# Kernel optimization log

Measured on AMD Instinct MI355X. Metric: run time of the kernel, lower is better.

The kernel has to match this reference:

```python
import jax, jax.numpy as jnp
import numpy as np

B, GRID, WIDTH, NBLOCKS = 128, 32, 100, 50  # num_layers=100 -> 50 two-GEMM residual blocks


def _forward(inputs, W0, Wa, Wb, b1, b2, b3, b4, mult, Wout, bout):
    Bb, G = inputs.shape[0], inputs.shape[1]
    T = G // 2
    even = jnp.arange(0, G, 2)
    odd = even + 1
    idx = (even - 1) % G  # [(i-1) % G for even i]

    def patch(i1, i2):
        # gather axis1 then axis2 -> (B, T, T, 3, 3) flattened to (B*T*T, 9)
        return inputs[:, i1][:, :, i2].reshape(-1, 9)

    # order: right, left, up, down, center (matches tf.concat order)
    flat = jnp.concatenate([patch(odd, even), patch(idx, even), patch(even, odd),
                            patch(even, idx), patch(even, even)], axis=-1)  # (B*T*T, 45)

    x = jax.nn.relu(flat @ W0)  # (B*T*T, 100)

    def block(x, p):
        wa, wb, bb1, bb2, bb3, bb4, m = p
        x1 = (x + bb1) @ wa
        x1 = 2.0 * x1 + bb2          # x1 + bias_2 + x1
        x1 = jax.nn.relu(x1)
        x1 = 2.0 * x1 + bb3          # x1 + bias_3 + x1
        x1 = (x1 @ wb) * m
        x = jax.nn.relu(x + x1 + bb4)
        return x, None

    x, _ = jax.lax.scan(block, x, (Wa, Wb, b1, b2, b3, b4, mult))

    x = (x @ Wout + bout).reshape(Bb, T, T, 4)

    jp1 = (jnp.arange(T) + 1) % T
    jm1 = (jnp.arange(T) - 1) % T
    x0, x1c, x2, x3 = x[..., 0], x[..., 1], x[..., 2], x[..., 3]
    right_c = x0 / (x1c[:, jp1] + x0)
    left_c = x1c / (x1c + x0[:, jm1])
    up_c = x2 / (x2 + x3[:, :, jp1])
    down_c = x3 / (x2[:, :, jm1] + x3)

    # corner contributions from the original fine-grid stencils
    oo = inputs[:, odd][:, :, odd]    # odd-odd fine points (ru corner)
    oi = inputs[:, odd][:, :, idx]    # rd corner
    io = inputs[:, idx][:, :, odd]    # lu corner
    ii = inputs[:, idx][:, :, idx]    # ld corner
    ru = -(oo[..., 0, 0] + oo[..., 1, 0] * right_c + oo[..., 0, 1] * up_c) / oo[..., 1, 1]
    rd = -(oi[..., 0, 2] + oi[..., 1, 2] * right_c + oi[..., 0, 1] * down_c) / oi[..., 1, 1]
    lu = -(io[..., 2, 0] + io[..., 1, 0] * left_c + io[..., 2, 1] * up_c) / io[..., 1, 1]
    ld = -(ii[..., 2, 2] + ii[..., 1, 2] * left_c + ii[..., 2, 1] * down_c) / ii[..., 1, 1]

    ones = jnp.ones_like(down_c)
    first_row = jnp.stack([ld, left_c, lu], axis=-1)
    second_row = jnp.stack([down_c, ones, up_c], axis=-1)
    third_row = jnp.stack([rd, right_c, ru], axis=-1)
    out = jnp.stack([first_row, second_row, third_row], axis=0)  # (3, B, T, T, 3)
    return jnp.transpose(out, (1, 2, 3, 0, 4))  # (B, T, T, 3, 3)


def setup_inputs() -> dict:
    key = jax.random.key(0)
    ks = jax.random.split(key, 6)
    # positive stencil entries keep the corner divisions well-conditioned
    inputs = jax.random.uniform(ks[0], (B, GRID, GRID, 3, 3), jnp.float32) + 0.5
    W0 = jax.random.normal(ks[1], (45, WIDTH), jnp.float32) * np.float32(np.sqrt(2.0 / 45))
    Wa = jax.random.normal(ks[2], (NBLOCKS, WIDTH, WIDTH), jnp.float32) * np.float32(np.sqrt(2.0 / WIDTH))
    # original inits linear_{i+1} to zeros; small random keeps the baseline non-degenerate
    Wb = jax.random.normal(ks[3], (NBLOCKS, WIDTH, WIDTH), jnp.float32) * np.float32(0.01)
    b1 = jnp.zeros((NBLOCKS,), jnp.float32)
    b2 = jnp.zeros((NBLOCKS,), jnp.float32)
    b3 = jnp.zeros((NBLOCKS,), jnp.float32)
    b4 = jnp.zeros((NBLOCKS,), jnp.float32)
    mult = jnp.ones((NBLOCKS,), jnp.float32)
    Wout = jax.random.normal(ks[4], (WIDTH, 4), jnp.float32) * np.float32(0.05)
    bout = jnp.ones((4,), jnp.float32)  # keeps contribution denominators ~2 (stable)
    return {"inputs": inputs, "W0": W0, "Wa": Wa, "Wb": Wb, "b1": b1, "b2": b2,
            "b3": b3, "b4": b4, "mult": mult, "Wout": Wout, "bout": bout}


def reference(inputs, W0, Wa, Wb, b1, b2, b3, b4, mult, Wout, bout):
    return _forward(inputs, W0, Wa, Wb, b1, b2, b3, b4, mult, Wout, bout)
```

## Files before the change

### kernel.cpp

```cpp
#include <hip/hip_runtime.h>
#include <cstddef>

typedef _Float16 f16x8 __attribute__((ext_vector_type(8)));
typedef _Float16 f16x4 __attribute__((ext_vector_type(4)));
typedef float f32x4 __attribute__((ext_vector_type(4)));
typedef float f32x16 __attribute__((ext_vector_type(16)));

constexpr int BATCH = 128;
constexpr int T     = 16;
constexpr int ROWS  = BATCH * T * T;
constexpr int WID   = 100;
constexpr int NB    = 50;
constexpr int KP    = 128;
constexpr int KS    = 7;
constexpr int NP    = 128;
constexpr int RPW   = 64;
constexpr int WCH   = KS * 4 * 512;

__global__ __launch_bounds__(256) void prep_kernel(
    const float* __restrict__ Wa, const float* __restrict__ Wb,
    _Float16* __restrict__ whi, _Float16* __restrict__ wlo,
    float* __restrict__ csA) {
  const int bid = blockIdx.x;
  const int bk = bid >> 1, m = bid & 1;
  const float* src = (m ? Wb : Wa) + (size_t)bk * (WID * WID);
  _Float16* dh = whi + (size_t)bid * WCH;
  _Float16* dl = wlo + (size_t)bid * WCH;
  for (int e = threadIdx.x; e < WCH; e += 256) {
    const int i  = e & 7;
    const int L  = (e >> 3) & 63;
    const int ct = (e >> 9) & 3;
    const int ks = e >> 11;
    const int k  = 16 * ks + 8 * (L >> 5) + i;
    const int j  = 32 * ct + (L & 31);
    const float v = (k < WID && j < WID) ? src[k * WID + j] : 0.0f;
    const _Float16 hi = (_Float16)v;
    dh[e] = hi;
    dl[e] = (_Float16)(v - (float)hi);
  }
  if (!m) {
    for (int col = threadIdx.x; col < NP; col += 256) {
      float s = 0.0f;
      if (col < WID) {
        for (int k = 0; k < WID; ++k) s += src[k * WID + col];
      }
      csA[bk * NP + col] = s;
    }
  }
}

__global__ __launch_bounds__(256) void first_layer_kernel(
    const float* __restrict__ inp, const float* __restrict__ W0,
    float* __restrict__ x0) {
  __shared__ float w0s[45 * WID];
  for (int i = threadIdx.x; i < 45 * WID; i += 256) w0s[i] = W0[i];
  __syncthreads();

  const int rq  = threadIdx.x >> 2;
  const int cq  = threadIdx.x & 3;
  const int row = blockIdx.x * 64 + rq;
  const int b   = row >> 8;
  const int t1  = (row >> 4) & 15;
  const int t2  = row & 15;
  const int g1  = 2 * t1, g2 = 2 * t2;
  const int g1m = (g1 + 31) & 31, g2m = (g2 + 31) & 31;
  const float* base = inp + (size_t)b * (32 * 32 * 9);
  const float* p0 = base + ((g1 + 1) * 32 + g2) * 9;
  const float* p1 = base + (g1m * 32 + g2) * 9;
  const float* p2 = base + (g1 * 32 + (g2 + 1)) * 9;
  const float* p3 = base + (g1 * 32 + g2m) * 9;
  const float* p4 = base + (g1 * 32 + g2) * 9;

  float f[45];
#pragma unroll
  for (int qq = 0; qq < 9; ++qq) {
    f[qq]      = p0[qq];
    f[9 + qq]  = p1[qq];
    f[18 + qq] = p2[qq];
    f[27 + qq] = p3[qq];
    f[36 + qq] = p4[qq];
  }

  float acc[25];
#pragma unroll
  for (int j = 0; j < 25; ++j) acc[j] = 0.0f;
  const int j0 = cq * 25;
#pragma unroll
  for (int k = 0; k < 45; ++k) {
    const float fv = f[k];
#pragma unroll
    for (int j = 0; j < 25; ++j) acc[j] += fv * w0s[k * WID + j0 + j];
  }
  float* orow = x0 + (size_t)row * WID + j0;
#pragma unroll
  for (int j = 0; j < 25; ++j) orow[j] = fmaxf(acc[j], 0.0f);
}

__global__ __launch_bounds__(512, 2) void chain_kernel(
    float* __restrict__ x0,
    const _Float16* __restrict__ whi, const _Float16* __restrict__ wlo,
    const float* __restrict__ csA,
    const float* __restrict__ B1, const float* __restrict__ B2,
    const float* __restrict__ B3, const float* __restrict__ B4,
    const float* __restrict__ M) {
  __shared__ __align__(16) _Float16 xhs[RPW * KP];
  __shared__ __align__(16) _Float16 xls[RPW * KP];

  const int tid  = threadIdx.x;
  const int lane = tid & 63;
  const int uw   = __builtin_amdgcn_readfirstlane(tid >> 6);
  const int rt   = uw >> 2;
  const int ct   = uw & 3;
  const int jr   = lane & 31;
  const int kg   = lane >> 5;
  const int rbase = blockIdx.x * RPW;

  const int row_x = 32 * rt + jr;
  const int sw    = (row_x & 7) << 3;

  for (int i = tid; i < RPW * KP; i += 512) {
    const int row = i >> 7, k = i & 127;
    const float v = (k < WID) ? x0[(size_t)(rbase + row) * WID + k] : 0.0f;
    const _Float16 hi = (_Float16)v;
    const int a = row * KP + (k ^ ((row & 7) << 3));
    xhs[a] = hi;
    xls[a] = (_Float16)(v - (float)hi);
  }

  int j0g[4];
#pragma unroll
  for (int g = 0; g < 4; ++g) j0g[g] = 32 * ct + 4 * kg + 8 * g;

  f32x4 xres[4];
#pragma unroll
  for (int g = 0; g < 4; ++g) {
    if (j0g[g] <= WID - 4) {
      xres[g] = *(const f32x4*)&x0[(size_t)(rbase + row_x) * WID + j0g[g]];
    } else {
      xres[g] = (f32x4){0.f, 0.f, 0.f, 0.f};
    }
  }
  __syncthreads();

  f32x16 acc;

  auto kloop = [&](const int gidx) {
    const _Float16* gh = whi + (size_t)gidx * WCH + ct * 512;
    const _Float16* gl = wlo + (size_t)gidx * WCH + ct * 512;
#pragma unroll
    for (int ks = 0; ks < KS; ++ks) {
      const f16x8 wh = *(const f16x8*)&gh[ks * 2048 + lane * 8];
      const f16x8 wl = *(const f16x8*)&gl[ks * 2048 + lane * 8];
      const int off = row_x * KP + ((16 * ks + 8 * kg) ^ sw);
      const f16x8 xh = *(const f16x8*)&xhs[off];
      const f16x8 xl = *(const f16x8*)&xls[off];
      acc = __builtin_amdgcn_mfma_f32_32x32x16_f16(wh, xh, acc, 0, 0, 0);
      acc = __builtin_amdgcn_mfma_f32_32x32x16_f16(wl, xh, acc, 0, 0, 0);
      acc = __builtin_amdgcn_mfma_f32_32x32x16_f16(wh, xl, acc, 0, 0, 0);
    }
  };

  for (int bk = 0; bk < NB; ++bk) {
#pragma unroll
    for (int e = 0; e < 16; ++e) acc[e] = 0.0f;
    kloop(bk * 2);
    __syncthreads();
    {
      const float b1 = B1[bk], b2 = B2[bk], b3 = B3[bk];
#pragma unroll
      for (int g = 0; g < 4; ++g) {
        const f32x4 cs = *(const f32x4*)&csA[bk * NP + j0g[g]];
        f16x4 hv, lv;
#pragma unroll
        for (int r = 0; r < 4; ++r) {
          const float t = 2.0f * (acc[g * 4 + r] + b1 * cs[r]) + b2;
          const float v = 2.0f * fmaxf(t, 0.0f) + b3;
          const _Float16 hi = (_Float16)v;
          hv[r] = hi;
          lv[r] = (_Float16)(v - (float)hi);
        }
        const int a = row_x * KP + (j0g[g] ^ sw);
        *(f16x4*)&xhs[a] = hv;
        *(f16x4*)&xls[a] = lv;
      }
    }
    __syncthreads();

#pragma unroll
    for (int e = 0; e < 16; ++e) acc[e] = 0.0f;
    kloop(bk * 2 + 1);
    __syncthreads();
    {
      const float b4v = B4[bk], mm = M[bk];
#pragma unroll
      for (int g = 0; g < 4; ++g) {
        f16x4 hv, lv;
#pragma unroll
        for (int r = 0; r < 4; ++r) {
          const float xn = fmaxf(xres[g][r] + acc[g * 4 + r] * mm + b4v, 0.0f);
          xres[g][r] = xn;
          const _Float16 hi = (_Float16)xn;
          hv[r] = hi;
          lv[r] = (_Float16)(xn - (float)hi);
        }
        const int a = row_x * KP + (j0g[g] ^ sw);
        *(f16x4*)&xhs[a] = hv;
        *(f16x4*)&xls[a] = lv;
      }
    }
    __syncthreads();
  }

#pragma unroll
  for (int g = 0; g < 4; ++g) {
    if (j0g[g] <= WID - 4)
      *(f32x4*)&x0[(size_t)(rbase + row_x) * WID + j0g[g]] = xres[g];
  }
}

__global__ __launch_bounds__(256) void out_kernel(
    const float* __restrict__ inp, const float* __restrict__ x0,
    const float* __restrict__ Wout, const float* __restrict__ bout,
    float* __restrict__ out) {
  __shared__ float ys[256 * 4];
  __shared__ float wouts[WID * 4];
  __shared__ float bos[4];
  const int tid = threadIdx.x;
  const int b   = blockIdx.x;

  for (int i = tid; i < WID * 4; i += 256) wouts[i] = Wout[i];
  if (tid < 4) bos[tid] = bout[tid];
  __syncthreads();

  const int row = b * 256 + tid;
  const float* xr = x0 + (size_t)row * WID;
  float a0 = 0.f, a1 = 0.f, a2 = 0.f, a3 = 0.f;
#pragma unroll 4
  for (int k = 0; k < WID; ++k) {
    const float xv = xr[k];
    a0 += xv * wouts[k * 4 + 0];
    a1 += xv * wouts[k * 4 + 1];
    a2 += xv * wouts[k * 4 + 2];
    a3 += xv * wouts[k * 4 + 3];
  }
  ys[tid * 4 + 0] = a0 + bos[0];
  ys[tid * 4 + 1] = a1 + bos[1];
  ys[tid * 4 + 2] = a2 + bos[2];
  ys[tid * 4 + 3] = a3 + bos[3];
  __syncthreads();

  const int i = tid >> 4, j = tid & 15;
  const int ip1 = (i + 1) & 15, im1 = (i + 15) & 15;
  const int jp1 = (j + 1) & 15, jm1 = (j + 15) & 15;
  auto Y = [&](int a, int c, int comp) { return ys[(((a << 4) | c) << 2) + comp]; };
  const float y0 = Y(i, j, 0), y1 = Y(i, j, 1), y2 = Y(i, j, 2), y3 = Y(i, j, 3);
  const float right_c = y0 / (Y(ip1, j, 1) + y0);
  const float left_c  = y1 / (y1 + Y(im1, j, 0));
  const float up_c    = y2 / (y2 + Y(i, jp1, 3));
  const float down_c  = y3 / (Y(i, jm1, 2) + y3);

  const float* base = inp + (size_t)b * (32 * 32 * 9);
  const int g1 = 2 * i + 1, g1m = (2 * i + 31) & 31;
  const int g2 = 2 * j + 1, g2m = (2 * j + 31) & 31;
  const float* oo = base + (g1 * 32 + g2) * 9;
  const float* oi = base + (g1 * 32 + g2m) * 9;
  const float* io = base + (g1m * 32 + g2) * 9;
  const float* ii = base + (g1m * 32 + g2m) * 9;
  const float ru = -(oo[0] + oo[3] * right_c + oo[1] * up_c) / oo[4];
  const float rd = -(oi[2] + oi[5] * right_c + oi[1] * down_c) / oi[4];
  const float lu = -(io[6] + io[3] * left_c + io[7] * up_c) / io[4];
  const float ld = -(ii[8] + ii[5] * left_c + ii[7] * down_c) / ii[4];

  float* o = out + (size_t)row * 9;
  o[0] = ld;     o[1] = left_c;  o[2] = lu;
  o[3] = down_c; o[4] = 1.0f;    o[5] = up_c;
  o[6] = rd;     o[7] = right_c; o[8] = ru;
}

extern "C" void kernel_launch(void* const* d_in, const int* in_sizes, int n_in,
                              void* d_out, int out_size, void* d_ws, size_t ws_size,
                              hipStream_t stream) {
  const float* inp  = (const float*)d_in[0];
  const float* W0   = (const float*)d_in[1];
  const float* Wa   = (const float*)d_in[2];
  const float* Wb   = (const float*)d_in[3];
  const float* B1   = (const float*)d_in[4];
  const float* B2   = (const float*)d_in[5];
  const float* B3   = (const float*)d_in[6];
  const float* B4   = (const float*)d_in[7];
  const float* M    = (const float*)d_in[8];
  const float* Wout = (const float*)d_in[9];
  const float* bout = (const float*)d_in[10];
  float* out = (float*)d_out;

  float* ws     = (float*)d_ws;
  float* x0     = ws;
  _Float16* whi = (_Float16*)(ws + 3276800);
  _Float16* wlo = (_Float16*)(ws + 3276800 + 716800);
  float* csA    = ws + 3276800 + 716800 + 716800;

  hipLaunchKernelGGL(prep_kernel, dim3(100), dim3(256), 0, stream,
                     Wa, Wb, whi, wlo, csA);
  hipLaunchKernelGGL(first_layer_kernel, dim3(ROWS / 64), dim3(256), 0, stream,
                     inp, W0, x0);
  hipLaunchKernelGGL(chain_kernel, dim3(ROWS / RPW), dim3(512), 0, stream,
                     x0, whi, wlo, csA, B1, B2, B3, B4, M);
  hipLaunchKernelGGL(out_kernel, dim3(BATCH), dim3(256), 0, stream,
                     inp, x0, Wout, bout, out);
}
```

Baseline: 337.2 us.

## Double-buffer LDS activations to drop barriers and prefetch weights per k-loop

Adds a second pair of LDS buffers so the intermediate activation of each residual block is written to separate storage, which removes the barrier that previously separated each GEMM from its epilogue write. All weight fragments for a k-loop are now loaded into registers before the MFMAs, which raises register pressure. The LDS swizzle widens from 8 to 16 row phases to reduce bank conflicts. LDS use per block doubles, which may reduce occupancy under the 2-blocks-per-CU launch bound.

```diff
diff --git a/kernel.cpp b/kernel.cpp
--- a/kernel.cpp
+++ b/kernel.cpp
@@ -105,6 +105,8 @@
     const float* __restrict__ M) {
   __shared__ __align__(16) _Float16 xhs[RPW * KP];
   __shared__ __align__(16) _Float16 xls[RPW * KP];
+  __shared__ __align__(16) _Float16 vhs[RPW * KP];
+  __shared__ __align__(16) _Float16 vls[RPW * KP];
 
   const int tid  = threadIdx.x;
   const int lane = tid & 63;
@@ -116,13 +118,13 @@
   const int rbase = blockIdx.x * RPW;
 
   const int row_x = 32 * rt + jr;
-  const int sw    = (row_x & 7) << 3;
+  const int sw    = (row_x & 15) << 3;
 
   for (int i = tid; i < RPW * KP; i += 512) {
     const int row = i >> 7, k = i & 127;
     const float v = (k < WID) ? x0[(size_t)(rbase + row) * WID + k] : 0.0f;
     const _Float16 hi = (_Float16)v;
-    const int a = row * KP + (k ^ ((row & 7) << 3));
+    const int a = row * KP + (k ^ ((row & 15) << 3));
     xhs[a] = hi;
     xls[a] = (_Float16)(v - (float)hi);
   }
@@ -144,27 +146,32 @@
 
   f32x16 acc;
 
-  auto kloop = [&](const int gidx) {
+  auto kloop = [&](const int gidx,
+                   const _Float16* __restrict__ xhsrc,
+                   const _Float16* __restrict__ xlsrc) {
     const _Float16* gh = whi + (size_t)gidx * WCH + ct * 512;
     const _Float16* gl = wlo + (size_t)gidx * WCH + ct * 512;
+    f16x8 wh[KS], wl[KS];
 #pragma unroll
     for (int ks = 0; ks < KS; ++ks) {
-      const f16x8 wh = *(const f16x8*)&gh[ks * 2048 + lane * 8];
-      const f16x8 wl = *(const f16x8*)&gl[ks * 2048 + lane * 8];
+      wh[ks] = *(const f16x8*)&gh[ks * 2048 + lane * 8];
+      wl[ks] = *(const f16x8*)&gl[ks * 2048 + lane * 8];
+    }
+#pragma unroll
+    for (int ks = 0; ks < KS; ++ks) {
       const int off = row_x * KP + ((16 * ks + 8 * kg) ^ sw);
-      const f16x8 xh = *(const f16x8*)&xhs[off];
-      const f16x8 xl = *(const f16x8*)&xls[off];
-      acc = __builtin_amdgcn_mfma_f32_32x32x16_f16(wh, xh, acc, 0, 0, 0);
-      acc = __builtin_amdgcn_mfma_f32_32x32x16_f16(wl, xh, acc, 0, 0, 0);
-      acc = __builtin_amdgcn_mfma_f32_32x32x16_f16(wh, xl, acc, 0, 0, 0);
+      const f16x8 xh = *(const f16x8*)&xhsrc[off];
+      const f16x8 xl = *(const f16x8*)&xlsrc[off];
+      acc = __builtin_amdgcn_mfma_f32_32x32x16_f16(wh[ks], xh, acc, 0, 0, 0);
+      acc = __builtin_amdgcn_mfma_f32_32x32x16_f16(wl[ks], xh, acc, 0, 0, 0);
+      acc = __builtin_amdgcn_mfma_f32_32x32x16_f16(wh[ks], xl, acc, 0, 0, 0);
     }
   };
 
   for (int bk = 0; bk < NB; ++bk) {
 #pragma unroll
     for (int e = 0; e < 16; ++e) acc[e] = 0.0f;
-    kloop(bk * 2);
-    __syncthreads();
+    kloop(bk * 2, xhs, xls);
     {
       const float b1 = B1[bk], b2 = B2[bk], b3 = B3[bk];
 #pragma unroll
@@ -180,16 +187,15 @@
           lv[r] = (_Float16)(v - (float)hi);
         }
         const int a = row_x * KP + (j0g[g] ^ sw);
-        *(f16x4*)&xhs[a] = hv;
-        *(f16x4*)&xls[a] = lv;
+        *(f16x4*)&vhs[a] = hv;
+        *(f16x4*)&vls[a] = lv;
       }
     }
     __syncthreads();
 
 #pragma unroll
     for (int e = 0; e < 16; ++e) acc[e] = 0.0f;
-    kloop(bk * 2 + 1);
-    __syncthreads();
+    kloop(bk * 2 + 1, vhs, vls);
     {
       const float b4v = B4[bk], mm = M[bk];
 #pragma unroll
```

After: 328.3 us (median of 2 runs). 1.03x faster.
